# Kernel optimization log

Measured on AMD Instinct MI355X. Metric: run time of the kernel, lower is better.

## Reference

```python
import jax, jax.numpy as jnp
import numpy as np

B, D, L, Q, E, NB, NI = 32, 16, 512, 8, 128, 30, 100000
BN_EPS = 1e-3  # tf.layers.batch_normalization default epsilon
LO, HI = 0.001, 1.0  # histogram_fixed_width value_range
_BN_INV = 1.0 / np.sqrt(1.0 + BN_EPS)  # inference BN with moving_mean=0, moving_var=1


def _bn(x, g, b):
    return g * (x * np.float32(_BN_INV)) + b


def setup_inputs() -> dict:
    key = jax.random.key(0)
    ks = jax.random.split(key, 16)
    dims = [NB, 128, 64, 32, 1]
    inp = {
        "doc": jax.random.randint(ks[0], (B, D, L), 0, NI, dtype=jnp.int32),
        "query": jax.random.randint(ks[1], (B, Q), 0, NI, dtype=jnp.int32),
        "item_embedding": jax.random.normal(ks[2], (NI, E), dtype=jnp.float32),
        "idf_table": jax.random.uniform(ks[3], (NI, 1), dtype=jnp.float32),
        "w_gate": jax.random.normal(ks[4], (Q,), dtype=jnp.float32),
        "g_in": jnp.ones((NB,), jnp.float32),
        "b_in": jnp.zeros((NB,), jnp.float32),
    }
    for i in range(4):
        fan_in, fan_out = dims[i], dims[i + 1]
        kW = jax.random.fold_in(ks[5], i)
        inp[f"W{i}"] = jax.random.normal(kW, (fan_in, fan_out), dtype=jnp.float32) / np.float32(np.sqrt(fan_in))
        inp[f"b{i}"] = jnp.zeros((fan_out,), jnp.float32)
        inp[f"g{i}"] = jnp.ones((fan_out,), jnp.float32)
        inp[f"be{i}"] = jnp.zeros((fan_out,), jnp.float32)
    return inp


def reference(doc, query, item_embedding, idf_table, w_gate, g_in, b_in,
              W0, b0, g0, be0, W1, b1, g1, be1, W2, b2, g2, be2, W3, b3, g3, be3):
    # Embedding lookups
    doc_vec = item_embedding[doc].reshape(B, D * L, E)      # [B, D*L, E]
    q_vec = item_embedding[query]                            # [B, Q, E]
    q_idf = idf_table[query][..., 0]                         # [B, Q]

    # Term gating network: softmax(w * idf) over query terms
    gate = jax.nn.softmax(w_gate * q_idf, axis=-1)           # [B, Q]

    # Cosine similarity of every doc token vs every query term
    d_norm = jnp.sqrt(jnp.sum(doc_vec * doc_vec, axis=-1))   # [B, D*L]
    q_norm = jnp.sqrt(jnp.sum(q_vec * q_vec, axis=-1))       # [B, Q]
    dots = jnp.einsum('bne,bqe->bqn', doc_vec, q_vec)        # [B, Q, D*L]
    sims = dots / (d_norm[:, None, :] * q_norm[:, :, None] + 1e-8)

    # Matching histogram: tf.histogram_fixed_width([0.001, 1], nbins) semantics
    idx = jnp.clip(jnp.floor((sims - LO) / (HI - LO) * NB).astype(jnp.int32), 0, NB - 1)
    rows = B * Q * D
    flat = (jnp.arange(rows, dtype=jnp.int32)[:, None] * NB + idx.reshape(rows, L)).reshape(-1)
    hist = jax.ops.segment_sum(jnp.ones((rows * L,), jnp.float32), flat,
                               num_segments=rows * NB).reshape(B, Q, D, NB)

    # DeepNet: BN -> [dense -> BN -> tanh] x 4 (dropout off at inference)
    x = _bn(hist, g_in, b_in)
    for W, b, g, be in ((W0, b0, g0, be0), (W1, b1, g1, be1),
                        (W2, b2, g2, be2), (W3, b3, g3, be3)):
        x = jnp.tanh(_bn(x @ W + b, g, be))
    query_out = x[..., 0]                                    # [B, Q, D]

    # Score aggregation over query terms
    return jnp.sum(query_out * gate[:, :, None], axis=1)     # [B, D]
```

## Files before the change

kernel.cpp:

```cpp
#include <hip/hip_runtime.h>
#include <math.h>


#define BN_INV 0.99950037468777346f

__device__ __forceinline__ float shflx(float v, int m) {
    return __shfl_xor(v, m, 64);
}

__device__ __forceinline__ int sel8i(int v0, int v1, int v2, int v3,
                                     int v4, int v5, int v6, int v7, int i) {
    int a0 = (i & 1) ? v1 : v0;
    int a1 = (i & 1) ? v3 : v2;
    int a2 = (i & 1) ? v5 : v4;
    int a3 = (i & 1) ? v7 : v6;
    int b0 = (i & 2) ? a1 : a0;
    int b1 = (i & 2) ? a3 : a2;
    return (i & 4) ? b1 : b0;
}

__device__ __forceinline__ float tanh_fast(float x) {
    float y = fminf(fmaxf(x, -9.0f), 9.0f);
    float t = exp2f(y * 2.8853901817f);
    return (t - 1.0f) * __builtin_amdgcn_rcpf(t + 1.0f);
}

template <bool PARTIAL>
__global__ __launch_bounds__(256, 4)
void drmm_hist(const int* __restrict__ doc,
               const int* __restrict__ query,
               const float* __restrict__ emb,
               float* __restrict__ hist_out)
{
    __shared__ float histw[4][8][32];
    __shared__ float qn_s[8];

    const int tid  = threadIdx.x;
    const int bid  = blockIdx.x;
    const int bd   = bid >> 1;
    const int b    = bid >> 5;
    const int wid  = tid >> 6;
    const int lane = tid & 63;

    for (int i = tid; i < 4 * 8 * 32; i += 256) ((float*)histw)[i] = 0.0f;

    const int* qrow = query + b * 8;
    const int qi0 = __builtin_amdgcn_readfirstlane(qrow[0]);
    const int qi1 = __builtin_amdgcn_readfirstlane(qrow[1]);
    const int qi2 = __builtin_amdgcn_readfirstlane(qrow[2]);
    const int qi3 = __builtin_amdgcn_readfirstlane(qrow[3]);
    const int qi4 = __builtin_amdgcn_readfirstlane(qrow[4]);
    const int qi5 = __builtin_amdgcn_readfirstlane(qrow[5]);
    const int qi6 = __builtin_amdgcn_readfirstlane(qrow[6]);
    const int qi7 = __builtin_amdgcn_readfirstlane(qrow[7]);

    const float4* qf0 = (const float4*)(emb + (size_t)qi0 * 128);
    const float4* qf1 = (const float4*)(emb + (size_t)qi1 * 128);
    const float4* qf2 = (const float4*)(emb + (size_t)qi2 * 128);
    const float4* qf3 = (const float4*)(emb + (size_t)qi3 * 128);
    const float4* qf4 = (const float4*)(emb + (size_t)qi4 * 128);
    const float4* qf5 = (const float4*)(emb + (size_t)qi5 * 128);
    const float4* qf6 = (const float4*)(emb + (size_t)qi6 * 128);
    const float4* qf7 = (const float4*)(emb + (size_t)qi7 * 128);

    if (wid == 0) {
        int q = lane >> 3, j = lane & 7;
        int qis = sel8i(qi0, qi1, qi2, qi3, qi4, qi5, qi6, qi7, q);
        const float4* qq = (const float4*)(emb + (size_t)qis * 128) + j * 4;
        float s = 0.f;
#pragma unroll
        for (int c = 0; c < 4; ++c) {
            float4 x = qq[c];
            s = fmaf(x.x, x.x, s); s = fmaf(x.y, x.y, s);
            s = fmaf(x.z, x.z, s); s = fmaf(x.w, x.w, s);
        }
        s += shflx(s, 1); s += shflx(s, 2); s += shflx(s, 4);
        if (j == 0) qn_s[q] = sqrtf(s);
    }
    __syncthreads();

    const int gtok = bid * 256 + tid;
    const int idx  = doc[gtok];
    const float4* rp = (const float4*)(emb + (size_t)idx * 128);

    float dd = 0.f;
    float dq0 = 0.f, dq1 = 0.f, dq2 = 0.f, dq3 = 0.f;
    float dq4 = 0.f, dq5 = 0.f, dq6 = 0.f, dq7 = 0.f;

    float4 vb[8];
#pragma unroll
    for (int p = 0; p < 8; ++p) vb[p] = rp[p];

#pragma unroll
    for (int c = 0; c < 4; ++c) {
        float4 nb[8];
        if (c < 3) {
#pragma unroll
            for (int p = 0; p < 8; ++p) nb[p] = rp[(c + 1) * 8 + p];
        }
#pragma unroll
        for (int p = 0; p < 8; ++p) {
            const int s = c * 8 + p;
            float4 v  = vb[p];
            float4 a0 = qf0[s], a1 = qf1[s], a2 = qf2[s], a3 = qf3[s];
            float4 a4 = qf4[s], a5 = qf5[s], a6 = qf6[s], a7 = qf7[s];
            dd  = fmaf(v.x, v.x, dd);  dd  = fmaf(v.y, v.y, dd);
            dd  = fmaf(v.z, v.z, dd);  dd  = fmaf(v.w, v.w, dd);
#define ACC(A, Dq) Dq = fmaf(v.x, A.x, Dq); Dq = fmaf(v.y, A.y, Dq); \
                   Dq = fmaf(v.z, A.z, Dq); Dq = fmaf(v.w, A.w, Dq);
            ACC(a0, dq0) ACC(a1, dq1) ACC(a2, dq2) ACC(a3, dq3)
            ACC(a4, dq4) ACC(a5, dq5) ACC(a6, dq6) ACC(a7, dq7)
#undef ACC
        }
        if (c < 3) {
#pragma unroll
            for (int p = 0; p < 8; ++p) vb[p] = nb[p];
        }
    }

    const float dn = sqrtf(dd);
#define DOBIN(J, DQ) {                                                  \
        float sim = DQ / (dn * qn_s[J] + 1e-8f);                        \
        float u = (sim - 0.001f) / 0.999f * 30.0f;                      \
        int bin = (int)floorf(u);                                       \
        bin = bin < 0 ? 0 : (bin > 29 ? 29 : bin);                      \
        atomicAdd(&histw[wid][J][bin], 1.0f);                           \
    }
    DOBIN(0, dq0) DOBIN(1, dq1) DOBIN(2, dq2) DOBIN(3, dq3)
    DOBIN(4, dq4) DOBIN(5, dq5) DOBIN(6, dq6) DOBIN(7, dq7)
#undef DOBIN
    __syncthreads();

    if (tid < 240) {
        int q = tid / 30, k = tid - q * 30;
        float s = histw[0][q][k] + histw[1][q][k]
                + histw[2][q][k] + histw[3][q][k];
        if (PARTIAL) {
            hist_out[(size_t)bid * 240 + tid] = s;
        } else {
            atomicAdd(&hist_out[bd * 240 + tid], s);
        }
    }
}

template <bool PARTIAL>
__global__ __launch_bounds__(512, 4)
void drmm_mlp(const float* __restrict__ hist_g,
              const int* __restrict__ query,
              const float* __restrict__ idf,
              const float* __restrict__ w_gate,
              const float* __restrict__ g_in, const float* __restrict__ b_in,
              const float* __restrict__ W0, const float* __restrict__ b0,
              const float* __restrict__ g0, const float* __restrict__ be0,
              const float* __restrict__ W1, const float* __restrict__ b1,
              const float* __restrict__ g1, const float* __restrict__ be1,
              const float* __restrict__ W2, const float* __restrict__ b2,
              const float* __restrict__ g2, const float* __restrict__ be2,
              const float* __restrict__ W3, const float* __restrict__ b3,
              const float* __restrict__ g3, const float* __restrict__ be3,
              float* __restrict__ out)
{
    __shared__ float xrow[8][30];
    __shared__ float h1s[8][128];
    __shared__ float h2s[8][64];
    __shared__ float h3s[8][32];
    __shared__ float gate_s[8];
    __shared__ float part[8];

    const int tid  = threadIdx.x;
    const int bd   = blockIdx.x;
    const int b    = bd >> 4;
    const int wid  = tid >> 6;
    const int lane = tid & 63;

    if (tid >= 504) {
        int q = tid - 504;
        float z = w_gate[q] * idf[query[b * 8 + q]];
        float m = z;
        m = fmaxf(m, shflx(m, 1)); m = fmaxf(m, shflx(m, 2)); m = fmaxf(m, shflx(m, 4));
        float e = expf(z - m);
        float s = e;
        s += shflx(s, 1); s += shflx(s, 2); s += shflx(s, 4);
        gate_s[q] = e / s;
    }

    if (tid < 240) {
        int q = tid / 30, k = tid - q * 30;
        float s;
        if (PARTIAL) {
            const float* hp = hist_g + (size_t)bd * 480 + tid;
            s = hp[0] + hp[240];
        } else {
            s = hist_g[bd * 240 + tid];
        }
        xrow[q][k] = g_in[k] * (s * BN_INV) + b_in[k];
    }
    __syncthreads();

    {
        float a0 = 0.f, a1 = 0.f;
#pragma unroll
        for (int k = 0; k < 30; ++k) {
            float xk = xrow[wid][k];
            a0 += xk * W0[k * 128 + lane];
            a1 += xk * W0[k * 128 + 64 + lane];
        }
        a0 += b0[lane]; a1 += b0[lane + 64];
        h1s[wid][lane]      = tanh_fast(g0[lane]      * (a0 * BN_INV) + be0[lane]);
        h1s[wid][lane + 64] = tanh_fast(g0[lane + 64] * (a1 * BN_INV) + be0[lane + 64]);
    }
    __syncthreads();

    {
        float a = 0.f;
#pragma unroll 8
        for (int k = 0; k < 128; ++k) a += h1s[wid][k] * W1[k * 64 + lane];
        a += b1[lane];
        h2s[wid][lane] = tanh_fast(g1[lane] * (a * BN_INV) + be1[lane]);
    }
    __syncthreads();

    if (lane < 32) {
        float a = 0.f;
#pragma unroll 8
        for (int k = 0; k < 64; ++k) a += h2s[wid][k] * W2[k * 32 + lane];
        a += b2[lane];
        h3s[wid][lane] = tanh_fast(g2[lane] * (a * BN_INV) + be2[lane]);
    }
    __syncthreads();

    if (lane == 0) {
        float a = 0.f;
#pragma unroll
        for (int k = 0; k < 32; ++k) a += h3s[wid][k] * W3[k];
        a += b3[0];
        float y = tanh_fast(g3[0] * (a * BN_INV) + be3[0]);
        part[wid] = gate_s[wid] * y;
    }
    __syncthreads();

    if (tid == 0) {
        float s = 0.f;
#pragma unroll
        for (int q = 0; q < 8; ++q) s += part[q];
        out[bd] = s;
    }
}

extern "C" void kernel_launch(void* const* d_in, const int* in_sizes, int n_in,
                              void* d_out, int out_size, void* d_ws, size_t ws_size,
                              hipStream_t stream) {
    (void)in_sizes; (void)n_in; (void)out_size;
    const int*   doc    = (const int*)d_in[0];
    const int*   query  = (const int*)d_in[1];
    const float* emb    = (const float*)d_in[2];
    const float* idf    = (const float*)d_in[3];
    const float* w_gate = (const float*)d_in[4];
    const float* g_in   = (const float*)d_in[5];
    const float* b_in   = (const float*)d_in[6];
    const float* W0  = (const float*)d_in[7];
    const float* b0  = (const float*)d_in[8];
    const float* g0  = (const float*)d_in[9];
    const float* be0 = (const float*)d_in[10];
    const float* W1  = (const float*)d_in[11];
    const float* b1  = (const float*)d_in[12];
    const float* g1  = (const float*)d_in[13];
    const float* be1 = (const float*)d_in[14];
    const float* W2  = (const float*)d_in[15];
    const float* b2  = (const float*)d_in[16];
    const float* g2  = (const float*)d_in[17];
    const float* be2 = (const float*)d_in[18];
    const float* W3  = (const float*)d_in[19];
    const float* b3  = (const float*)d_in[20];
    const float* g3  = (const float*)d_in[21];
    const float* be3 = (const float*)d_in[22];

    float* hist_g = (float*)d_ws;
    const size_t need_partial = (size_t)1024 * 240 * sizeof(float);

    if (ws_size >= need_partial) {
        drmm_hist<true><<<dim3(1024), dim3(256), 0, stream>>>(doc, query, emb, hist_g);
        drmm_mlp<true><<<dim3(512), dim3(512), 0, stream>>>(
            hist_g, query, idf, w_gate, g_in, b_in,
            W0, b0, g0, be0, W1, b1, g1, be1,
            W2, b2, g2, be2, W3, b3, g3, be3, (float*)d_out);
    } else {
        hipMemsetAsync(hist_g, 0, 512 * 240 * sizeof(float), stream);
        drmm_hist<false><<<dim3(1024), dim3(256), 0, stream>>>(doc, query, emb, hist_g);
        drmm_mlp<false><<<dim3(512), dim3(512), 0, stream>>>(
            hist_g, query, idf, w_gate, g_in, b_in,
            W0, b0, g0, be0, W1, b1, g1, be1,
            W2, b2, g2, be2, W3, b3, g3, be3, (float*)d_out);
    }
}
```

Baseline: 50.69 us.

## Split each doc token's embedding dot products across two lanes

Each doc token is now handled by a pair of lanes, and each lane covers half of the 128-dim embedding. The partial sums are combined with an xor-shuffle, and each lane then bins four of the eight query terms. The grid doubles to 2048 blocks, launch bounds ask for 8 blocks per CU, and the MLP kernel sums four partial histograms per row instead of two. The aim is more parallelism and memory-level concurrency for the gather-bound embedding reads and less per-thread serial work, at the cost of extra shuffles, double the partial-histogram traffic and tighter register limits.

```diff
diff --git a/kernel.cpp b/kernel.cpp
--- a/kernel.cpp
+++ b/kernel.cpp
@@ -25,8 +25,12 @@
     return (t - 1.0f) * __builtin_amdgcn_rcpf(t + 1.0f);
 }
 
+__device__ __forceinline__ float4 ld4(const float* base, int elem_off) {
+    return *(const float4*)(base + elem_off);
+}
+
 template <bool PARTIAL>
-__global__ __launch_bounds__(256, 4)
+__global__ __launch_bounds__(256, 8)
 void drmm_hist(const int* __restrict__ doc,
                const int* __restrict__ query,
                const float* __restrict__ emb,
@@ -37,10 +41,10 @@
 
     const int tid  = threadIdx.x;
     const int bid  = blockIdx.x;
-    const int bd   = bid >> 1;
-    const int b    = bid >> 5;
+    const int b    = bid >> 6;
     const int wid  = tid >> 6;
     const int lane = tid & 63;
+    const int half = tid & 1;
 
     for (int i = tid; i < 4 * 8 * 32; i += 256) ((float*)histw)[i] = 0.0f;
 
@@ -54,14 +58,14 @@
     const int qi6 = __builtin_amdgcn_readfirstlane(qrow[6]);
     const int qi7 = __builtin_amdgcn_readfirstlane(qrow[7]);
 
-    const float4* qf0 = (const float4*)(emb + (size_t)qi0 * 128);
-    const float4* qf1 = (const float4*)(emb + (size_t)qi1 * 128);
-    const float4* qf2 = (const float4*)(emb + (size_t)qi2 * 128);
-    const float4* qf3 = (const float4*)(emb + (size_t)qi3 * 128);
-    const float4* qf4 = (const float4*)(emb + (size_t)qi4 * 128);
-    const float4* qf5 = (const float4*)(emb + (size_t)qi5 * 128);
-    const float4* qf6 = (const float4*)(emb + (size_t)qi6 * 128);
-    const float4* qf7 = (const float4*)(emb + (size_t)qi7 * 128);
+    const float* qb0 = emb + (size_t)qi0 * 128;
+    const float* qb1 = emb + (size_t)qi1 * 128;
+    const float* qb2 = emb + (size_t)qi2 * 128;
+    const float* qb3 = emb + (size_t)qi3 * 128;
+    const float* qb4 = emb + (size_t)qi4 * 128;
+    const float* qb5 = emb + (size_t)qi5 * 128;
+    const float* qb6 = emb + (size_t)qi6 * 128;
+    const float* qb7 = emb + (size_t)qi7 * 128;
 
     if (wid == 0) {
         int q = lane >> 3, j = lane & 7;
@@ -79,9 +83,10 @@
     }
     __syncthreads();
 
-    const int gtok = bid * 256 + tid;
+    const int gtok = bid * 128 + (tid >> 1);
     const int idx  = doc[gtok];
-    const float4* rp = (const float4*)(emb + (size_t)idx * 128);
+    const int hoff = half * 64;
+    const float* rbase = emb + (size_t)idx * 128;
 
     float dd = 0.f;
     float dq0 = 0.f, dq1 = 0.f, dq2 = 0.f, dq3 = 0.f;
@@ -89,21 +94,23 @@
 
     float4 vb[8];
 #pragma unroll
-    for (int p = 0; p < 8; ++p) vb[p] = rp[p];
-
-#pragma unroll
-    for (int c = 0; c < 4; ++c) {
+    for (int p = 0; p < 8; ++p) vb[p] = ld4(rbase, hoff + p * 4);
+
+#pragma unroll
+    for (int c = 0; c < 2; ++c) {
         float4 nb[8];
-        if (c < 3) {
-#pragma unroll
-            for (int p = 0; p < 8; ++p) nb[p] = rp[(c + 1) * 8 + p];
+        if (c < 1) {
+#pragma unroll
+            for (int p = 0; p < 8; ++p) nb[p] = ld4(rbase, hoff + (8 + p) * 4);
         }
 #pragma unroll
         for (int p = 0; p < 8; ++p) {
-            const int s = c * 8 + p;
+            const int eo = hoff + (c * 8 + p) * 4;
             float4 v  = vb[p];
-            float4 a0 = qf0[s], a1 = qf1[s], a2 = qf2[s], a3 = qf3[s];
-            float4 a4 = qf4[s], a5 = qf5[s], a6 = qf6[s], a7 = qf7[s];
+            float4 a0 = ld4(qb0, eo), a1 = ld4(qb1, eo);
+            float4 a2 = ld4(qb2, eo), a3 = ld4(qb3, eo);
+            float4 a4 = ld4(qb4, eo), a5 = ld4(qb5, eo);
+            float4 a6 = ld4(qb6, eo), a7 = ld4(qb7, eo);
             dd  = fmaf(v.x, v.x, dd);  dd  = fmaf(v.y, v.y, dd);
             dd  = fmaf(v.z, v.z, dd);  dd  = fmaf(v.w, v.w, dd);
 #define ACC(A, Dq) Dq = fmaf(v.x, A.x, Dq); Dq = fmaf(v.y, A.y, Dq); \
@@ -112,11 +119,17 @@
             ACC(a4, dq4) ACC(a5, dq5) ACC(a6, dq6) ACC(a7, dq7)
 #undef ACC
         }
-        if (c < 3) {
+        if (c < 1) {
 #pragma unroll
             for (int p = 0; p < 8; ++p) vb[p] = nb[p];
         }
     }
+
+    dd  += shflx(dd, 1);
+    dq0 += shflx(dq0, 1); dq1 += shflx(dq1, 1);
+    dq2 += shflx(dq2, 1); dq3 += shflx(dq3, 1);
+    dq4 += shflx(dq4, 1); dq5 += shflx(dq5, 1);
+    dq6 += shflx(dq6, 1); dq7 += shflx(dq7, 1);
 
     const float dn = sqrtf(dd);
 #define DOBIN(J, DQ) {                                                  \
@@ -126,8 +139,11 @@
         bin = bin < 0 ? 0 : (bin > 29 ? 29 : bin);                      \
         atomicAdd(&histw[wid][J][bin], 1.0f);                           \
     }
-    DOBIN(0, dq0) DOBIN(1, dq1) DOBIN(2, dq2) DOBIN(3, dq3)
-    DOBIN(4, dq4) DOBIN(5, dq5) DOBIN(6, dq6) DOBIN(7, dq7)
+    if (half == 0) {
+        DOBIN(0, dq0) DOBIN(1, dq1) DOBIN(2, dq2) DOBIN(3, dq3)
+    } else {
+        DOBIN(4, dq4) DOBIN(5, dq5) DOBIN(6, dq6) DOBIN(7, dq7)
+    }
 #undef DOBIN
     __syncthreads();
 
@@ -138,7 +154,7 @@
         if (PARTIAL) {
             hist_out[(size_t)bid * 240 + tid] = s;
         } else {
-            atomicAdd(&hist_out[bd * 240 + tid], s);
+            atomicAdd(&hist_out[(bid >> 2) * 240 + tid], s);
         }
     }
 }
@@ -188,8 +204,8 @@
         int q = tid / 30, k = tid - q * 30;
         float s;
         if (PARTIAL) {
-            const float* hp = hist_g + (size_t)bd * 480 + tid;
-            s = hp[0] + hp[240];
+            const float* hp = hist_g + (size_t)bd * 960 + tid;
+            s = (hp[0] + hp[240]) + (hp[480] + hp[720]);
         } else {
             s = hist_g[bd * 240 + tid];
         }
@@ -276,17 +292,17 @@
     const float* be3 = (const float*)d_in[22];
 
     float* hist_g = (float*)d_ws;
-    const size_t need_partial = (size_t)1024 * 240 * sizeof(float);
+    const size_t need_partial = (size_t)2048 * 240 * sizeof(float);
 
     if (ws_size >= need_partial) {
-        drmm_hist<true><<<dim3(1024), dim3(256), 0, stream>>>(doc, query, emb, hist_g);
+        drmm_hist<true><<<dim3(2048), dim3(256), 0, stream>>>(doc, query, emb, hist_g);
         drmm_mlp<true><<<dim3(512), dim3(512), 0, stream>>>(
             hist_g, query, idf, w_gate, g_in, b_in,
             W0, b0, g0, be0, W1, b1, g1, be1,
             W2, b2, g2, be2, W3, b3, g3, be3, (float*)d_out);
     } else {
         hipMemsetAsync(hist_g, 0, 512 * 240 * sizeof(float), stream);
-        drmm_hist<false><<<dim3(1024), dim3(256), 0, stream>>>(doc, query, emb, hist_g);
+        drmm_hist<false><<<dim3(2048), dim3(256), 0, stream>>>(doc, query, emb, hist_g);
         drmm_mlp<false><<<dim3(512), dim3(512), 0, stream>>>(
             hist_g, query, idf, w_gate, g_in, b_in,
             W0, b0, g0, be0, W1, b1, g1, be1,
```

Result: slower. 106.1 us (+109.3%).

## Stage query embeddings in LDS and double-buffer doc row loads

Applied to the files above, without the earlier changes.

Each block now loads the eight query embedding rows into shared memory once. The inner dot-product loop reads them from LDS instead of issuing repeated global loads per step. The doc index load moves to the start of the kernel, and the doc row is streamed through two register buffers, with empty asm pins to enforce prefetch ordering. A barrier between two stages that run in the same wave is removed. The LDS broadcast reads and higher register pressure could offset the savings in global query traffic.

```diff
diff --git a/kernel.cpp b/kernel.cpp
--- a/kernel.cpp
+++ b/kernel.cpp
@@ -25,6 +25,8 @@
     return (t - 1.0f) * __builtin_amdgcn_rcpf(t + 1.0f);
 }
 
+#define PIN4(V) asm volatile("" : "+v"((V).x), "+v"((V).y), "+v"((V).z), "+v"((V).w))
+
 template <bool PARTIAL>
 __global__ __launch_bounds__(256, 4)
 void drmm_hist(const int* __restrict__ doc,
@@ -34,6 +36,7 @@
 {
     __shared__ float histw[4][8][32];
     __shared__ float qn_s[8];
+    __shared__ float4 qlds[8][32];
 
     const int tid  = threadIdx.x;
     const int bid  = blockIdx.x;
@@ -41,6 +44,9 @@
     const int b    = bid >> 5;
     const int wid  = tid >> 6;
     const int lane = tid & 63;
+
+    const int gtok = bid * 256 + tid;
+    const int idx  = doc[gtok];
 
     for (int i = tid; i < 4 * 8 * 32; i += 256) ((float*)histw)[i] = 0.0f;
 
@@ -54,19 +60,17 @@
     const int qi6 = __builtin_amdgcn_readfirstlane(qrow[6]);
     const int qi7 = __builtin_amdgcn_readfirstlane(qrow[7]);
 
-    const float4* qf0 = (const float4*)(emb + (size_t)qi0 * 128);
-    const float4* qf1 = (const float4*)(emb + (size_t)qi1 * 128);
-    const float4* qf2 = (const float4*)(emb + (size_t)qi2 * 128);
-    const float4* qf3 = (const float4*)(emb + (size_t)qi3 * 128);
-    const float4* qf4 = (const float4*)(emb + (size_t)qi4 * 128);
-    const float4* qf5 = (const float4*)(emb + (size_t)qi5 * 128);
-    const float4* qf6 = (const float4*)(emb + (size_t)qi6 * 128);
-    const float4* qf7 = (const float4*)(emb + (size_t)qi7 * 128);
+    {
+        int q = tid >> 5;
+        int c = tid & 31;
+        int qis = sel8i(qi0, qi1, qi2, qi3, qi4, qi5, qi6, qi7, q);
+        qlds[q][c] = *((const float4*)(emb + (size_t)qis * 128) + c);
+    }
 
     if (wid == 0) {
-        int q = lane >> 3, j = lane & 7;
+        int q = lane >> 3, jj = lane & 7;
         int qis = sel8i(qi0, qi1, qi2, qi3, qi4, qi5, qi6, qi7, q);
-        const float4* qq = (const float4*)(emb + (size_t)qis * 128) + j * 4;
+        const float4* qq = (const float4*)(emb + (size_t)qis * 128) + jj * 4;
         float s = 0.f;
 #pragma unroll
         for (int c = 0; c < 4; ++c) {
@@ -75,48 +79,68 @@
             s = fmaf(x.z, x.z, s); s = fmaf(x.w, x.w, s);
         }
         s += shflx(s, 1); s += shflx(s, 2); s += shflx(s, 4);
-        if (j == 0) qn_s[q] = sqrtf(s);
-    }
-    __syncthreads();
-
-    const int gtok = bid * 256 + tid;
-    const int idx  = doc[gtok];
+        if (jj == 0) qn_s[q] = sqrtf(s);
+    }
+    __syncthreads();
+
     const float4* rp = (const float4*)(emb + (size_t)idx * 128);
 
     float dd = 0.f;
     float dq0 = 0.f, dq1 = 0.f, dq2 = 0.f, dq3 = 0.f;
     float dq4 = 0.f, dq5 = 0.f, dq6 = 0.f, dq7 = 0.f;
 
-    float4 vb[8];
-#pragma unroll
-    for (int p = 0; p < 8; ++p) vb[p] = rp[p];
-
-#pragma unroll
-    for (int c = 0; c < 4; ++c) {
-        float4 nb[8];
-        if (c < 3) {
-#pragma unroll
-            for (int p = 0; p < 8; ++p) nb[p] = rp[(c + 1) * 8 + p];
-        }
-#pragma unroll
-        for (int p = 0; p < 8; ++p) {
-            const int s = c * 8 + p;
-            float4 v  = vb[p];
-            float4 a0 = qf0[s], a1 = qf1[s], a2 = qf2[s], a3 = qf3[s];
-            float4 a4 = qf4[s], a5 = qf5[s], a6 = qf6[s], a7 = qf7[s];
-            dd  = fmaf(v.x, v.x, dd);  dd  = fmaf(v.y, v.y, dd);
-            dd  = fmaf(v.z, v.z, dd);  dd  = fmaf(v.w, v.w, dd);
-#define ACC(A, Dq) Dq = fmaf(v.x, A.x, Dq); Dq = fmaf(v.y, A.y, Dq); \
-                   Dq = fmaf(v.z, A.z, Dq); Dq = fmaf(v.w, A.w, Dq);
-            ACC(a0, dq0) ACC(a1, dq1) ACC(a2, dq2) ACC(a3, dq3)
-            ACC(a4, dq4) ACC(a5, dq5) ACC(a6, dq6) ACC(a7, dq7)
-#undef ACC
-        }
-        if (c < 3) {
-#pragma unroll
-            for (int p = 0; p < 8; ++p) vb[p] = nb[p];
-        }
-    }
+#define CSTEP(V, S) {                                                       \
+        float4 v  = (V);                                                    \
+        float4 a0 = qlds[0][S], a1 = qlds[1][S];                            \
+        float4 a2 = qlds[2][S], a3 = qlds[3][S];                            \
+        float4 a4 = qlds[4][S], a5 = qlds[5][S];                            \
+        float4 a6 = qlds[6][S], a7 = qlds[7][S];                            \
+        dd = fmaf(v.x, v.x, dd); dd = fmaf(v.y, v.y, dd);                   \
+        dd = fmaf(v.z, v.z, dd); dd = fmaf(v.w, v.w, dd);                   \
+        dq0 = fmaf(v.x, a0.x, dq0); dq0 = fmaf(v.y, a0.y, dq0);             \
+        dq0 = fmaf(v.z, a0.z, dq0); dq0 = fmaf(v.w, a0.w, dq0);             \
+        dq1 = fmaf(v.x, a1.x, dq1); dq1 = fmaf(v.y, a1.y, dq1);             \
+        dq1 = fmaf(v.z, a1.z, dq1); dq1 = fmaf(v.w, a1.w, dq1);             \
+        dq2 = fmaf(v.x, a2.x, dq2); dq2 = fmaf(v.y, a2.y, dq2);             \
+        dq2 = fmaf(v.z, a2.z, dq2); dq2 = fmaf(v.w, a2.w, dq2);             \
+        dq3 = fmaf(v.x, a3.x, dq3); dq3 = fmaf(v.y, a3.y, dq3);             \
+        dq3 = fmaf(v.z, a3.z, dq3); dq3 = fmaf(v.w, a3.w, dq3);             \
+        dq4 = fmaf(v.x, a4.x, dq4); dq4 = fmaf(v.y, a4.y, dq4);             \
+        dq4 = fmaf(v.z, a4.z, dq4); dq4 = fmaf(v.w, a4.w, dq4);             \
+        dq5 = fmaf(v.x, a5.x, dq5); dq5 = fmaf(v.y, a5.y, dq5);             \
+        dq5 = fmaf(v.z, a5.z, dq5); dq5 = fmaf(v.w, a5.w, dq5);             \
+        dq6 = fmaf(v.x, a6.x, dq6); dq6 = fmaf(v.y, a6.y, dq6);             \
+        dq6 = fmaf(v.z, a6.z, dq6); dq6 = fmaf(v.w, a6.w, dq6);             \
+        dq7 = fmaf(v.x, a7.x, dq7); dq7 = fmaf(v.y, a7.y, dq7);             \
+        dq7 = fmaf(v.z, a7.z, dq7); dq7 = fmaf(v.w, a7.w, dq7);             \
+    }
+
+    float4 A[8], B[8];
+#pragma unroll
+    for (int p = 0; p < 8; ++p) A[p] = rp[p];
+#pragma unroll
+    for (int p = 0; p < 8; ++p) B[p] = rp[8 + p];
+#pragma unroll
+    for (int p = 0; p < 8; ++p) PIN4(A[p]);
+#pragma unroll
+    for (int p = 0; p < 8; ++p) CSTEP(A[p], p)
+#pragma unroll
+    for (int p = 0; p < 8; ++p) A[p] = rp[16 + p];
+#pragma unroll
+    for (int p = 0; p < 8; ++p) PIN4(B[p]);
+#pragma unroll
+    for (int p = 0; p < 8; ++p) CSTEP(B[p], 8 + p)
+#pragma unroll
+    for (int p = 0; p < 8; ++p) B[p] = rp[24 + p];
+#pragma unroll
+    for (int p = 0; p < 8; ++p) PIN4(A[p]);
+#pragma unroll
+    for (int p = 0; p < 8; ++p) CSTEP(A[p], 16 + p)
+#pragma unroll
+    for (int p = 0; p < 8; ++p) PIN4(B[p]);
+#pragma unroll
+    for (int p = 0; p < 8; ++p) CSTEP(B[p], 24 + p)
+#undef CSTEP
 
     const float dn = sqrtf(dd);
 #define DOBIN(J, DQ) {                                                  \
@@ -227,7 +251,6 @@
         a += b2[lane];
         h3s[wid][lane] = tanh_fast(g2[lane] * (a * BN_INV) + be2[lane]);
     }
-    __syncthreads();
 
     if (lane == 0) {
         float a = 0.f;
```

After: 47.62 us. 6.1% less time.
